# Optimization experiments

Measured on AMD Instinct MI355X. Metric: run time of the kernel, lower is better.

## Reference

```python
import jax, jax.numpy as jnp
import numpy as np

BATCH = 65536
INPUT_DIM = 128
NUM_PROTOTYPES = 512
OUTPUT_DIM = 8


def setup_inputs() -> dict:
    key = jax.random.key(0)
    k1, k2, k3 = jax.random.split(key, 3)
    x = jax.random.normal(k1, (BATCH, INPUT_DIM), dtype=jnp.float32)
    prototypes = jax.random.normal(k2, (NUM_PROTOTYPES, INPUT_DIM), dtype=jnp.float32)
    prototype_outputs = jax.random.normal(k3, (NUM_PROTOTYPES, OUTPUT_DIM), dtype=jnp.float32)
    relevance = jnp.ones((INPUT_DIM,), dtype=jnp.float32)
    return {"x": x, "prototypes": prototypes, "prototype_outputs": prototype_outputs, "relevance": relevance}


def reference(x, prototypes, prototype_outputs, relevance):
    # dist[b,p] = sum_d r2[d] * (x[b,d] - proto[p,d])^2
    # Expanded to avoid materializing the (B, P, D) broadcast tensor:
    #   = sum_d r2*x^2 + sum_d r2*p^2 - 2 * sum_d x * r2 * p
    r2 = relevance ** 2                                   # [D]
    x_sq = (x * x) @ r2                                   # [B]
    p_sq = (prototypes * prototypes) @ r2                 # [P]
    cross = x @ (prototypes * r2).T                       # [B, P]
    dist = x_sq[:, None] + p_sq[None, :] - 2.0 * cross    # [B, P]
    idx = jnp.argmin(dist, axis=1)                        # [B]
    return prototype_outputs[idx]                         # [B, output_dim]
```

## Files before the change

### kernel.cpp

```cpp
#include <hip/hip_runtime.h>

#define BATCH 65536
#define DIM 128
#define NPROTO 512
#define ODIM 8

#define ROWS 64
#define THREADS 512
#define XSTRIDE 132


__global__ void grlvq_prep(const float* __restrict__ proto,
                           const float* __restrict__ rel,
                           float* __restrict__ wT,
                           float* __restrict__ psq) {
    int p = blockIdx.x * blockDim.x + threadIdx.x;
    if (p >= NPROTO) return;
    const int wb = p >> 6, oo = (p >> 3) & 7, j = p & 7;
    float acc = 0.f;
    #pragma unroll 8
    for (int d = 0; d < DIM; ++d) {
        float r = rel[d];
        float r2 = r * r;
        float v = proto[p * DIM + d];
        wT[wb * 8192 + oo * 1024 + (d >> 2) * 32 + j * 4 + (d & 3)] = v * r2;
        acc = fmaf(r2 * v, v, acc);
    }
    psq[p] = acc;
}

__global__ __launch_bounds__(THREADS, 8) void grlvq_main(const float* __restrict__ x,
                                                         const float* __restrict__ wT,
                                                         const float* __restrict__ psq,
                                                         const float* __restrict__ pout,
                                                         float* __restrict__ out) {
    __shared__ float xs[ROWS * XSTRIDE];
    __shared__ float red_s[ROWS * 8];
    __shared__ int   red_i[ROWS * 8];

    const int t = threadIdx.x;
    const int rowBase = blockIdx.x * ROWS;

    #pragma unroll
    for (int k = 0; k < 4; ++k) {
        const int idx = t + k * THREADS;
        const int r = idx >> 5, c = idx & 31;
        float4 v = *(const float4*)(x + (size_t)(rowBase + r) * DIM + c * 4);
        *(float4*)(&xs[r * XSTRIDE + c * 4]) = v;
    }
    __syncthreads();

    const int lane = t & 63;
    const int wid  = __builtin_amdgcn_readfirstlane(t >> 6);
    const float* xrow  = &xs[lane * XSTRIDE];
    const float* wbase = wT + (size_t)wid * 8192;
    const int pbase = wid * 64;

    float best = INFINITY;
    int bestIdx = pbase;

    #pragma unroll 1
    for (int oo = 0; oo < 8; ++oo) {
        float acc[8];
        #pragma unroll
        for (int j = 0; j < 8; ++j) acc[j] = 0.f;

        const float* wp = wbase + oo * 1024;
        #pragma unroll 4
        for (int c = 0; c < 32; ++c) {
            float4 xv = *(const float4*)(xrow + c * 4);
            const float* wc = wp + c * 32;
            #pragma unroll
            for (int j = 0; j < 8; ++j) {
                acc[j] = fmaf(xv.x, wc[j * 4 + 0], acc[j]);
                acc[j] = fmaf(xv.y, wc[j * 4 + 1], acc[j]);
                acc[j] = fmaf(xv.z, wc[j * 4 + 2], acc[j]);
                acc[j] = fmaf(xv.w, wc[j * 4 + 3], acc[j]);
            }
        }

        #pragma unroll
        for (int j = 0; j < 8; ++j) {
            float s = psq[pbase + oo * 8 + j] - 2.0f * acc[j];
            if (s < best) { best = s; bestIdx = pbase + oo * 8 + j; }
        }
    }

    red_s[lane * 8 + wid] = best;
    red_i[lane * 8 + wid] = bestIdx;
    __syncthreads();

    if (t < ROWS) {
        float b = INFINITY;
        int bi = 0;
        #pragma unroll
        for (int w8 = 0; w8 < 8; ++w8) {
            float s = red_s[t * 8 + w8];
            int  id = red_i[t * 8 + w8];
            if (s < b) { b = s; bi = id; }
        }
        const float4* po = (const float4*)(pout + (size_t)bi * ODIM);
        float4* op = (float4*)(out + (size_t)(rowBase + t) * ODIM);
        op[0] = po[0];
        op[1] = po[1];
    }
}

extern "C" void kernel_launch(void* const* d_in, const int* in_sizes, int n_in,
                              void* d_out, int out_size, void* d_ws, size_t ws_size,
                              hipStream_t stream) {
    const float* x     = (const float*)d_in[0];
    const float* proto = (const float*)d_in[1];
    const float* pout  = (const float*)d_in[2];
    const float* rel   = (const float*)d_in[3];
    float* out = (float*)d_out;

    float* wT  = (float*)d_ws;
    float* psq = wT + NPROTO * DIM;

    grlvq_prep<<<(NPROTO + 127) / 128, 128, 0, stream>>>(proto, rel, wT, psq);
    grlvq_main<<<BATCH / ROWS, THREADS, 0, stream>>>(x, wT, psq, pout, out);
}
```

Before: 202.5 us.

## Process two rows per lane with transposed shared x tile to reuse weight loads

Each block now handles 128 rows, and each lane computes distances for two rows at once. The scalar, wave-uniform prototype weights are reused across both rows, halving weight load traffic per FMA. The x tile is stored column-major in shared memory as float4 so lane reads are contiguous, and that buffer is reused for the reduction arrays. The prep kernel is vectorized with float4 loads and stores. In exchange, register use doubles for the accumulators, occupancy is lowered to 4 blocks, and there are only 512 blocks, which may underfill the GPU.

```diff
diff --git a/kernel.cpp b/kernel.cpp
--- a/kernel.cpp
+++ b/kernel.cpp
@@ -5,9 +5,8 @@
 #define NPROTO 512
 #define ODIM 8
 
-#define ROWS 64
+#define ROWS 128
 #define THREADS 512
-#define XSTRIDE 132
 
 
 __global__ void grlvq_prep(const float* __restrict__ proto,
@@ -17,77 +16,97 @@
     int p = blockIdx.x * blockDim.x + threadIdx.x;
     if (p >= NPROTO) return;
     const int wb = p >> 6, oo = (p >> 3) & 7, j = p & 7;
+    float* wout = wT + wb * 8192 + oo * 1024 + j * 4;
     float acc = 0.f;
     #pragma unroll 8
-    for (int d = 0; d < DIM; ++d) {
-        float r = rel[d];
-        float r2 = r * r;
-        float v = proto[p * DIM + d];
-        wT[wb * 8192 + oo * 1024 + (d >> 2) * 32 + j * 4 + (d & 3)] = v * r2;
-        acc = fmaf(r2 * v, v, acc);
+    for (int c = 0; c < 32; ++c) {
+        float4 rv = *(const float4*)(rel + c * 4);
+        float4 pv = *(const float4*)(proto + (size_t)p * DIM + c * 4);
+        float4 o;
+        float r2;
+        r2 = rv.x * rv.x; o.x = pv.x * r2; acc = fmaf(r2 * pv.x, pv.x, acc);
+        r2 = rv.y * rv.y; o.y = pv.y * r2; acc = fmaf(r2 * pv.y, pv.y, acc);
+        r2 = rv.z * rv.z; o.z = pv.z * r2; acc = fmaf(r2 * pv.z, pv.z, acc);
+        r2 = rv.w * rv.w; o.w = pv.w * r2; acc = fmaf(r2 * pv.w, pv.w, acc);
+        *(float4*)(wout + c * 32) = o;
     }
     psq[p] = acc;
 }
 
-__global__ __launch_bounds__(THREADS, 8) void grlvq_main(const float* __restrict__ x,
+__global__ __launch_bounds__(THREADS, 4) void grlvq_main(const float* __restrict__ x,
                                                          const float* __restrict__ wT,
                                                          const float* __restrict__ psq,
                                                          const float* __restrict__ pout,
                                                          float* __restrict__ out) {
-    __shared__ float xs[ROWS * XSTRIDE];
-    __shared__ float red_s[ROWS * 8];
-    __shared__ int   red_i[ROWS * 8];
+    __shared__ __align__(16) char smem[65536];
+    float4* xs4  = (float4*)smem;
+    float*  red_s = (float*)smem;
+    int*    red_i = (int*)(smem + 4096);
 
     const int t = threadIdx.x;
     const int rowBase = blockIdx.x * ROWS;
 
-    #pragma unroll
-    for (int k = 0; k < 4; ++k) {
-        const int idx = t + k * THREADS;
-        const int r = idx >> 5, c = idx & 31;
-        float4 v = *(const float4*)(x + (size_t)(rowBase + r) * DIM + c * 4);
-        *(float4*)(&xs[r * XSTRIDE + c * 4]) = v;
+    {
+        const int r = t & 127;
+        const int cbase = t >> 7;
+        const float4* xg = (const float4*)(x + (size_t)(rowBase + r) * DIM);
+        #pragma unroll
+        for (int k = 0; k < 8; ++k) {
+            const int c = cbase + 4 * k;
+            xs4[c * 128 + r] = xg[c];
+        }
     }
     __syncthreads();
 
     const int lane = t & 63;
     const int wid  = __builtin_amdgcn_readfirstlane(t >> 6);
-    const float* xrow  = &xs[lane * XSTRIDE];
     const float* wbase = wT + (size_t)wid * 8192;
     const int pbase = wid * 64;
 
-    float best = INFINITY;
-    int bestIdx = pbase;
+    float bestA = INFINITY, bestB = INFINITY;
+    int idxA = pbase, idxB = pbase;
 
     #pragma unroll 1
     for (int oo = 0; oo < 8; ++oo) {
-        float acc[8];
+        float accA[8], accB[8];
         #pragma unroll
-        for (int j = 0; j < 8; ++j) acc[j] = 0.f;
+        for (int j = 0; j < 8; ++j) { accA[j] = 0.f; accB[j] = 0.f; }
 
         const float* wp = wbase + oo * 1024;
         #pragma unroll 4
         for (int c = 0; c < 32; ++c) {
-            float4 xv = *(const float4*)(xrow + c * 4);
+            float4 xa = xs4[c * 128 + lane];
+            float4 xb = xs4[c * 128 + lane + 64];
             const float* wc = wp + c * 32;
             #pragma unroll
             for (int j = 0; j < 8; ++j) {
-                acc[j] = fmaf(xv.x, wc[j * 4 + 0], acc[j]);
-                acc[j] = fmaf(xv.y, wc[j * 4 + 1], acc[j]);
-                acc[j] = fmaf(xv.z, wc[j * 4 + 2], acc[j]);
-                acc[j] = fmaf(xv.w, wc[j * 4 + 3], acc[j]);
+                float w0 = wc[j * 4 + 0], w1 = wc[j * 4 + 1];
+                float w2 = wc[j * 4 + 2], w3 = wc[j * 4 + 3];
+                accA[j] = fmaf(xa.x, w0, accA[j]);
+                accA[j] = fmaf(xa.y, w1, accA[j]);
+                accA[j] = fmaf(xa.z, w2, accA[j]);
+                accA[j] = fmaf(xa.w, w3, accA[j]);
+                accB[j] = fmaf(xb.x, w0, accB[j]);
+                accB[j] = fmaf(xb.y, w1, accB[j]);
+                accB[j] = fmaf(xb.z, w2, accB[j]);
+                accB[j] = fmaf(xb.w, w3, accB[j]);
             }
         }
 
         #pragma unroll
         for (int j = 0; j < 8; ++j) {
-            float s = psq[pbase + oo * 8 + j] - 2.0f * acc[j];
-            if (s < best) { best = s; bestIdx = pbase + oo * 8 + j; }
+            float pq = psq[pbase + oo * 8 + j];
+            float sA = pq - 2.0f * accA[j];
+            float sB = pq - 2.0f * accB[j];
+            if (sA < bestA) { bestA = sA; idxA = pbase + oo * 8 + j; }
+            if (sB < bestB) { bestB = sB; idxB = pbase + oo * 8 + j; }
         }
     }
 
-    red_s[lane * 8 + wid] = best;
-    red_i[lane * 8 + wid] = bestIdx;
+    __syncthreads();
+
+    red_s[lane * 8 + wid] = bestA;        red_i[lane * 8 + wid] = idxA;
+    red_s[(lane + 64) * 8 + wid] = bestB; red_i[(lane + 64) * 8 + wid] = idxB;
     __syncthreads();
 
     if (t < ROWS) {
@@ -118,6 +137,6 @@
     float* wT  = (float*)d_ws;
     float* psq = wT + NPROTO * DIM;
 
-    grlvq_prep<<<(NPROTO + 127) / 128, 128, 0, stream>>>(proto, rel, wT, psq);
+    grlvq_prep<<<2, 256, 0, stream>>>(proto, rel, wT, psq);
     grlvq_main<<<BATCH / ROWS, THREADS, 0, stream>>>(x, wT, psq, pout, out);
 }
```

Result: faster. 178.3 us (-11.9%).
